# Kernel tuning notes

Measured on AMD Instinct MI355X. Metric: run time of the kernel, lower is better.

The kernel has to match this reference:

```python
import jax, jax.numpy as jnp
import numpy as np
from math import factorial

# ---------- real Clebsch-Gordan coefficients (numpy, computed once) ----------

def _cg(j1, m1, j2, m2, j3, m3):
    if m1 + m2 != m3 or not (abs(j1 - j2) <= j3 <= j1 + j2):
        return 0.0
    f = factorial
    pref = ((2 * j3 + 1) * f(j3 + j1 - j2) * f(j3 - j1 + j2) * f(j1 + j2 - j3) / f(j1 + j2 + j3 + 1)) ** 0.5
    pref *= (f(j3 + m3) * f(j3 - m3) * f(j1 - m1) * f(j1 + m1) * f(j2 - m2) * f(j2 + m2)) ** 0.5
    s = 0.0
    for k in range(0, j1 + j2 + j3 + 1):
        dn = [j1 + j2 - j3 - k, j1 - m1 - k, j2 + m2 - k, j3 - j2 + m1 + k, j3 - j1 - m2 + k]
        if any(t < 0 for t in dn):
            continue
        s += (-1) ** k / (f(k) * f(dn[0]) * f(dn[1]) * f(dn[2]) * f(dn[3]) * f(dn[4]))
    return pref * s

def _U(l):
    # complex -> real spherical-harmonic change of basis, rows = real m (-l..l)
    u = np.zeros((2 * l + 1, 2 * l + 1), dtype=complex)
    s = 1.0 / np.sqrt(2.0)
    u[l, l] = 1.0
    for m in range(1, l + 1):
        u[l + m, l + m] = (-1) ** m * s
        u[l + m, l - m] = s
        u[l - m, l - m] = 1j * s
        u[l - m, l + m] = -1j * (-1) ** m * s
    return u

def _real_cg(l1, l2, l3):
    Cc = np.zeros((2 * l1 + 1, 2 * l2 + 1, 2 * l3 + 1), dtype=complex)
    for i, m1 in enumerate(range(-l1, l1 + 1)):
        for j, m2 in enumerate(range(-l2, l2 + 1)):
            for k, m3 in enumerate(range(-l3, l3 + 1)):
                Cc[i, j, k] = _cg(l1, m1, l2, m2, l3, m3)
    Cr = np.einsum('ia,jb,kc,abc->ijk', _U(l1), _U(l2), _U(l3).conj(), Cc)
    return np.real(Cr).astype(np.float32)

C110 = _real_cg(1, 1, 0); C220 = _real_cg(2, 2, 0)
C121 = _real_cg(1, 2, 1); C211 = _real_cg(2, 1, 1); C231 = _real_cg(2, 3, 1)
C112 = _real_cg(1, 1, 2); C132 = _real_cg(1, 3, 2); C222 = _real_cg(2, 2, 2)

N_NODE, N_EDGE, F, AVG = 5000, 50000, 64, 10.0


def setup_inputs() -> dict:
    key = jax.random.key(0)
    ks = jax.random.split(key, 20)
    nrm = lambda k, sh: jax.random.normal(k, sh, dtype=jnp.float32)
    return {
        'vectors': nrm(ks[0], (N_EDGE, 3)) * 0.25,  # keep lengths mostly < r_cut=1
        'node_feats': nrm(ks[1], (N_NODE, 9 * F)),   # 64x0e + 64x1o + 64x2e
        'node_specie': jnp.zeros((N_NODE,), jnp.int32),
        'senders': jax.random.randint(ks[2], (N_EDGE,), 0, N_NODE),
        'receivers': jax.random.randint(ks[3], (N_EDGE,), 0, N_NODE),
        'Wsc0': nrm(ks[4], (1, F, F)), 'Wsc1': nrm(ks[5], (1, F, F)), 'Wsc2': nrm(ks[6], (1, F, F)),
        'Wu0': nrm(ks[7], (F, F)), 'Wu1': nrm(ks[8], (F, F)), 'Wu2': nrm(ks[9], (F, F)),
        'Wm1': nrm(ks[10], (8, 64)), 'Wm2': nrm(ks[11], (64, 64)), 'Wm3': nrm(ks[12], (64, 13 * F)),
        'Wd0': nrm(ks[13], (3 * F, 3 * F)), 'Wd1': nrm(ks[14], (5 * F, F)), 'Wd2': nrm(ks[15], (5 * F, F)),
    }


def reference(vectors, node_feats, node_specie, senders, receivers,
              Wsc0, Wsc1, Wsc2, Wu0, Wu1, Wu2, Wm1, Wm2, Wm3, Wd0, Wd1, Wd2):
    N = node_feats.shape[0]
    # radial embedding: bessel(8) * poly_envelope(5,2)  (r_cut = 1)
    x = jnp.sqrt(jnp.maximum(jnp.sum(vectors ** 2, -1), 1e-12))  # [E]
    unit = vectors / x[:, None]
    n = jnp.arange(1, 9, dtype=vectors.dtype)
    basis = jnp.sqrt(2.0) * jnp.sin(jnp.pi * n[None, :] * x[:, None]) / x[:, None]  # [E,8]
    env = jnp.where(x < 1.0, 1.0 - 28 * x ** 6 + 48 * x ** 7 - 21 * x ** 8, 0.0)
    radial = basis * env[:, None]
    # spherical harmonics l=1..3, component normalization, m = -l..l
    ux, uy, uz = unit[:, 0], unit[:, 1], unit[:, 2]
    sh1 = (3.0 ** 0.5) * jnp.stack([uy, uz, ux], -1)
    s15, s5 = 15.0 ** 0.5, 5.0 ** 0.5
    sh2 = jnp.stack([s15 * ux * uy, s15 * uy * uz, 0.5 * s5 * (3 * uz ** 2 - 1), s15 * ux * uz, 0.5 * s15 * (ux ** 2 - uy ** 2)], -1)
    c35, c105, c21, c7 = (35.0 / 8) ** 0.5, 105.0 ** 0.5, (21.0 / 8) ** 0.5, (7.0 ** 0.5) / 2
    sh3 = jnp.stack([c35 * uy * (3 * ux ** 2 - uy ** 2), c105 * ux * uy * uz, c21 * uy * (5 * uz ** 2 - 1),
                     c7 * uz * (5 * uz ** 2 - 3), c21 * ux * (5 * uz ** 2 - 1), 0.5 * c105 * uz * (ux ** 2 - uy ** 2),
                     c35 * ux * (ux ** 2 - 3 * uy ** 2)], -1)
    # split node features into irrep blocks: [N,F], [N,F,3], [N,F,5]
    f0 = node_feats[:, :F]
    f1 = node_feats[:, F:4 * F].reshape(N, F, 3)
    f2 = node_feats[:, 4 * F:9 * F].reshape(N, F, 5)
    inv_f = 1.0 / F ** 0.5
    # species-indexed skip connection (on pre-linear_up features)
    sc0 = jnp.einsum('nf,nfg->ng', f0, Wsc0[node_specie]) * inv_f
    sc1 = jnp.einsum('nfc,nfg->ngc', f1, Wsc1[node_specie]) * inv_f
    sc2 = jnp.einsum('nfc,nfg->ngc', f2, Wsc2[node_specie]) * inv_f
    # linear_up (per-irrep channel mixing)
    g0 = (f0 @ Wu0) * inv_f
    g1 = jnp.einsum('nfc,fg->ngc', f1, Wu1) * inv_f
    g2 = jnp.einsum('nfc,fg->ngc', f2, Wu2) * inv_f
    # gather sender features onto edges
    s0, s1, s2 = g0[senders], g1[senders], g2[senders]
    tp = lambda feat, sh, C: jnp.einsum('efi,ej,ijk->efk', feat, sh, jnp.asarray(C))
    # messages = concat(filtered feats, CG tensor products filtered to 0e+1o+2e)
    m0 = jnp.concatenate([s0, tp(s1, sh1, C110)[..., 0], tp(s2, sh2, C220)[..., 0]], 1)            # [E,3F]
    m1 = jnp.concatenate([s1, s0[:, :, None] * sh1[:, None, :], tp(s1, sh2, C121),
                          tp(s2, sh1, C211), tp(s2, sh3, C231)], 1)                                   # [E,5F,3]
    m2 = jnp.concatenate([s2, s0[:, :, None] * sh2[:, None, :], tp(s1, sh1, C112),
                          tp(s1, sh3, C132), tp(s2, sh2, C222)], 1)                                   # [E,5F,5]
    # edge-wise scalar MLP on radial embedding -> one gain per message irrep (13F)
    h = jax.nn.swish(radial @ Wm1 / 8.0 ** 0.5)
    h = jax.nn.swish(h @ Wm2 / 64.0 ** 0.5)
    mix = h @ Wm3 / 64.0 ** 0.5                                                                        # [E,13F]
    m0 = m0 * mix[:, :3 * F]
    m1 = m1 * mix[:, 3 * F:8 * F, None]
    m2 = m2 * mix[:, 8 * F:13 * F, None]
    # scatter-add aggregation into receivers
    inv_avg = 1.0 / AVG ** 0.5
    a0 = jax.ops.segment_sum(m0, receivers, num_segments=N) * inv_avg
    a1 = jax.ops.segment_sum(m1, receivers, num_segments=N) * inv_avg
    a2 = jax.ops.segment_sum(m2, receivers, num_segments=N) * inv_avg
    # linear_down to 3F x0e (F feats + 2F gates) + F x1o + F x2e
    d0 = a0 @ Wd0 / (3 * F) ** 0.5
    d1 = jnp.einsum('nmc,mf->nfc', a1, Wd1) / (5 * F) ** 0.5
    d2 = jnp.einsum('nmc,mf->nfc', a2, Wd2) / (5 * F) ** 0.5
    # gate nonlinearity
    x0 = jax.nn.swish(d0[:, :F])
    gates = jax.nn.swish(d0[:, F:3 * F])
    o1 = d1 * gates[:, :F, None]
    o2 = d2 * gates[:, F:2 * F, None]
    return jnp.concatenate([x0 + sc0, (o1 + sc1).reshape(N, 3 * F), (o2 + sc2).reshape(N, 5 * F)], 1)
```

## Files before the change

### kernel.cpp

```cpp
#include <hip/hip_runtime.h>
#include <math.h>

#define CG110 0
#define CG220 9
#define CG121 34
#define CG211 79
#define CG231 124
#define CG112 229
#define CG132 274
#define CG222 379
#define CGTOT 504

__device__ double dfact(int n){ double r=1.0; for(int i=2;i<=n;i++) r*=(double)i; return r; }

__device__ double cg_coeff(int j1,int m1,int j2,int m2,int j3,int m3){
  if(m1+m2!=m3) return 0.0;
  int lo = j1>j2 ? j1-j2 : j2-j1;
  if(j3 < lo || j3 > j1+j2) return 0.0;
  double pref = sqrt((double)(2*j3+1)*dfact(j3+j1-j2)*dfact(j3-j1+j2)*dfact(j1+j2-j3)/dfact(j1+j2+j3+1));
  pref *= sqrt(dfact(j3+m3)*dfact(j3-m3)*dfact(j1-m1)*dfact(j1+m1)*dfact(j2-m2)*dfact(j2+m2));
  double s=0.0;
  for(int k=0;k<=j1+j2+j3;k++){
    int d0=j1+j2-j3-k, d1=j1-m1-k, d2=j2+m2-k, d3=j3-j2+m1+k, d4=j3-j1-m2+k;
    if(d0<0||d1<0||d2<0||d3<0||d4<0) continue;
    double term = 1.0/(dfact(k)*dfact(d0)*dfact(d1)*dfact(d2)*dfact(d3)*dfact(d4));
    s += (k&1)? -term : term;
  }
  return pref*s;
}

__device__ void u_elem(int l,int i,int a,double& re,double& im){
  const double s=0.70710678118654752440;
  re=0.0; im=0.0;
  int mi=i-l, ma=a-l;
  if(mi==0){ if(ma==0) re=1.0; }
  else if(mi>0){ if(ma==mi) re=(mi&1)?-s:s; else if(ma==-mi) re=s; }
  else { int m=-mi; if(ma==mi) im=s; else if(ma==-mi) im=(m&1)?s:-s; }
}

__device__ float real_cg_elem(int l1,int l2,int l3,int ii,int jj,int kk){
  double acc=0.0;
  int alist[2]={ii, 2*l1-ii}; int na=(alist[1]==alist[0])?1:2;
  int blist[2]={jj, 2*l2-jj}; int nb=(blist[1]==blist[0])?1:2;
  int clist[2]={kk, 2*l3-kk}; int nc=(clist[1]==clist[0])?1:2;
  for(int ai=0;ai<na;ai++) for(int bi=0;bi<nb;bi++) for(int ci=0;ci<nc;ci++){
    int a=alist[ai], b=blist[bi], c=clist[ci];
    double w = cg_coeff(l1,a-l1,l2,b-l2,l3,c-l3);
    if(w==0.0) continue;
    double u1r,u1i,u2r,u2i,u3r,u3i;
    u_elem(l1,ii,a,u1r,u1i); u_elem(l2,jj,b,u2r,u2i); u_elem(l3,kk,c,u3r,u3i);
    double ar = u1r*u2r - u1i*u2i;
    double aiv= u1r*u2i + u1i*u2r;
    acc += (ar*u3r + aiv*u3i)*w;
  }
  return (float)acc;
}

__global__ void cg_init_kernel(float* __restrict__ cgbuf){
  int tid = blockIdx.x*blockDim.x + threadIdx.x;
  if(tid>=CGTOT) return;
  const int l1s[8]={1,2,1,2,2,1,1,2};
  const int l2s[8]={1,2,2,1,3,1,3,2};
  const int l3s[8]={0,0,1,1,1,2,2,2};
  const int offs[9]={CG110,CG220,CG121,CG211,CG231,CG112,CG132,CG222,CGTOT};
  int t=0;
  for(int u=0;u<8;u++){ if(tid>=offs[u] && tid<offs[u+1]){ t=u; break; } }
  int l1=l1s[t], l2=l2s[t], l3=l3s[t];
  int rem = tid - offs[t];
  int d3=2*l3+1, d2=2*l2+1;
  int k = rem % d3; int j = (rem/d3)%d2; int i = rem/(d3*d2);
  cgbuf[tid] = real_cg_elem(l1,l2,l3,i,j,k);
}


__global__ __launch_bounds__(256) void node_linear_kernel(
    const float* __restrict__ node_feats, const int* __restrict__ specie,
    const float* __restrict__ Wsc0, const float* __restrict__ Wsc1, const float* __restrict__ Wsc2,
    const float* __restrict__ Wu0,  const float* __restrict__ Wu1,  const float* __restrict__ Wu2,
    float* __restrict__ g_packed, float* __restrict__ sc_packed, int N)
{
  __shared__ float feat[576];
  int n = blockIdx.x; if(n>=N) return;
  const float4* src = (const float4*)(node_feats + (size_t)n*576);
  float4* fd = (float4*)feat;
  for(int i=threadIdx.x;i<144;i+=256) fd[i]=src[i];
  __syncthreads();
  int sp = specie[n];
  const float inv_f = 0.125f;
  for(int o=threadIdx.x; o<1152; o+=256){
    int isSc = (o>=576);
    int p = o - (isSc?576:0);
    float acc=0.f;
    if(p<64){
      const float* W = isSc ? (Wsc0 + (size_t)sp*4096) : Wu0;
      #pragma unroll 8
      for(int f=0; f<64; f++) acc += feat[f]*W[f*64+p];
    } else if(p<256){
      int q=p-64; int f,c;
      if (isSc){ f=q/3; c=q-3*f; } else { c=q>>6; f=q&63; }
      const float* W = isSc ? (Wsc1 + (size_t)sp*4096) : Wu1;
      #pragma unroll 8
      for(int fp=0; fp<64; fp++) acc += feat[64+3*fp+c]*W[fp*64+f];
    } else {
      int q=p-256; int f,c;
      if (isSc){ f=q/5; c=q-5*f; } else { c=q>>6; f=q&63; }
      const float* W = isSc ? (Wsc2 + (size_t)sp*4096) : Wu2;
      #pragma unroll 8
      for(int fp=0; fp<64; fp++) acc += feat[256+5*fp+c]*W[fp*64+f];
    }
    float* dst = isSc ? sc_packed : g_packed;
    dst[(size_t)n*576 + p] = acc*inv_f;
  }
}

__global__ __launch_bounds__(256) void node_gemm_kernel(
  const float* __restrict__ node_feats,
  const float* __restrict__ Wsc0, const float* __restrict__ Wsc1, const float* __restrict__ Wsc2,
  const float* __restrict__ Wu0,  const float* __restrict__ Wu1,  const float* __restrict__ Wu2,
  float* __restrict__ g_packed, float* __restrict__ sc_packed, int N)
{
  __shared__ float As[64][17];
  __shared__ float Bs[16][64];
  int tid = threadIdx.x;
  int tx = tid & 15, ty = tid >> 4;
  int s = blockIdx.y;
  int n0 = blockIdx.x*64;

  int sub = s % 9;
  int isSc = (s >= 9);
  int abase, astride;
  const float* W;
  if (sub == 0){ abase = 0; astride = 1; W = isSc? Wsc0 : Wu0; }
  else if (sub < 4){ int c = sub-1; abase = 64+c; astride = 3; W = isSc? Wsc1 : Wu1; }
  else { int c = sub-4; abase = 256+c; astride = 5; W = isSc? Wsc2 : Wu2; }
  int obase, ostride;
  if (isSc){ obase = abase; ostride = astride; }
  else {
    if (sub==0){ obase=0; ostride=1; }
    else if (sub<4){ obase = 64+64*(sub-1); ostride=1; }
    else { obase = 256+64*(sub-4); ostride=1; }
  }
  float* dst = isSc ? sc_packed : g_packed;

  float acc[4][4];
  #pragma unroll
  for(int i=0;i<4;i++)
    #pragma unroll
    for(int j=0;j<4;j++) acc[i][j]=0.f;

  for (int k0=0; k0<64; k0+=16){
    #pragma unroll
    for (int l=0;l<4;l++){
      int idx = tid + l*256;
      int row = idx>>4, kk = idx&15;
      int n = n0+row;
      As[row][kk] = (n<N)? node_feats[(size_t)n*576 + abase + astride*(k0+kk)] : 0.f;
    }
    #pragma unroll
    for (int l=0;l<4;l++){
      int idx = tid + l*256;
      int kk = idx>>6, j = idx&63;
      Bs[kk][j] = W[(k0+kk)*64 + j];
    }
    __syncthreads();
    #pragma unroll
    for (int kk=0; kk<16; kk++){
      float av[4];
      #pragma unroll
      for(int i=0;i<4;i++) av[i] = As[ty*4+i][kk];
      float4 bv = *(const float4*)&Bs[kk][tx*4];
      #pragma unroll
      for(int i=0;i<4;i++){
        acc[i][0] += av[i]*bv.x; acc[i][1] += av[i]*bv.y;
        acc[i][2] += av[i]*bv.z; acc[i][3] += av[i]*bv.w;
      }
    }
    __syncthreads();
  }
  const float scale = 0.125f;
  #pragma unroll
  for(int i=0;i<4;i++){
    int n = n0 + ty*4+i;
    if (n>=N) continue;
    #pragma unroll
    for(int j=0;j<4;j++){
      int f = tx*4+j;
      dst[(size_t)n*576 + obase + ostride*f] = acc[i][j]*scale;
    }
  }
}

__global__ void count_kernel(const int* __restrict__ recv, int* __restrict__ counts, int E){
  int e = blockIdx.x*256 + threadIdx.x;
  if(e<E) atomicAdd(&counts[recv[e]],1);
}

__global__ __launch_bounds__(1024) void scan_kernel(const int* __restrict__ counts,
                                                    int* __restrict__ offsets,
                                                    int* __restrict__ cursor, int n){
  __shared__ int tmp[1024];
  int tid = threadIdx.x;
  int per = (n + 1023)/1024;
  int base = tid*per;
  int s = 0;
  for(int i=0;i<per;i++){ int idx=base+i; if(idx<n) s += counts[idx]; }
  tmp[tid]=s; __syncthreads();
  for(int off=1; off<1024; off<<=1){
    int v = (tid>=off)? tmp[tid-off] : 0;
    __syncthreads();
    tmp[tid]+=v;
    __syncthreads();
  }
  int run = (tid==0)? 0 : tmp[tid-1];
  for(int i=0;i<per;i++){
    int idx=base+i;
    if(idx<n){ offsets[idx]=run; cursor[idx]=run; run += counts[idx]; }
  }
  if(tid==1023) offsets[n]=tmp[1023];
}

__global__ void scatter_kernel(const int* __restrict__ recv, int* __restrict__ cursor,
                               int* __restrict__ edge_list, int E){
  int e = blockIdx.x*256 + threadIdx.x;
  if(e<E){ int pos=atomicAdd(&cursor[recv[e]],1); edge_list[pos]=e; }
}

__global__ __launch_bounds__(256) void geom_kernel(
  const float* __restrict__ vectors, const int* __restrict__ edge_list,
  const int* __restrict__ senders,
  float* __restrict__ radbuf, float* __restrict__ shbuf, int* __restrict__ spos, int E)
{
  int pos = blockIdx.x*256 + threadIdx.x;
  if (pos >= E) return;
  int e = edge_list[pos];
  spos[pos] = senders[e];
  float vx=vectors[e*3], vy=vectors[e*3+1], vz=vectors[e*3+2];
  float x2 = vx*vx+vy*vy+vz*vz;
  float x  = sqrtf(fmaxf(x2, 1e-12f));
  float inv= 1.f/x;
  float ux=vx*inv, uy=vy*inv, uz=vz*inv;
  float env = 0.f;
  if(x<1.f){
    float x3=x*x*x; float x6=x3*x3; float x7=x6*x; float x8=x7*x;
    env = 1.f-28.f*x6+48.f*x7-21.f*x8;
  }
  float* rb = radbuf + (size_t)pos*8;
  #pragma unroll
  for(int nn=1;nn<=8;nn++)
    rb[nn-1] = 1.4142135623730951f * sinf(3.14159265358979323846f*(float)nn*x)*inv*env;
  float sh[16];
  const float s3=1.7320508075688772f;
  sh[0]=s3*uy; sh[1]=s3*uz; sh[2]=s3*ux;
  const float s15=3.872983346207417f, s5=2.23606797749979f;
  sh[3]=s15*ux*uy; sh[4]=s15*uy*uz;
  sh[5]=0.5f*s5*(3.f*uz*uz-1.f);
  sh[6]=s15*ux*uz; sh[7]=0.5f*s15*(ux*ux-uy*uy);
  const float c35=2.091650066335189f, c105=10.246950765959598f;
  const float c21=1.620185174601965f, c7=1.3228756555322954f;
  sh[8] =c35*uy*(3.f*ux*ux-uy*uy);
  sh[9] =c105*ux*uy*uz;
  sh[10]=c21*uy*(5.f*uz*uz-1.f);
  sh[11]=c7*uz*(5.f*uz*uz-3.f);
  sh[12]=c21*ux*(5.f*uz*uz-1.f);
  sh[13]=0.5f*c105*uz*(ux*ux-uy*uy);
  sh[14]=c35*ux*(ux*ux-3.f*uy*uy);
  sh[15]=0.f;
  float* sb = shbuf + (size_t)pos*16;
  #pragma unroll
  for(int k=0;k<16;k++) sb[k]=sh[k];
}

__global__ __launch_bounds__(256) void wtab_kernel(
  const float* __restrict__ shbuf, const float* __restrict__ cgbuf,
  float* __restrict__ wtabbuf, int E)
{
  __shared__ float cgs[504];
  for(int i=threadIdx.x;i<504;i+=256) cgs[i]=cgbuf[i];
  __syncthreads();
  long long t = (long long)blockIdx.x*256 + threadIdx.x;
  if (t >= (long long)E*104) return;
  int pos = (int)(t/104), idx = (int)(t - (long long)pos*104);
  const float* sh = shbuf + (size_t)pos*16;
  float v = 0.f;
  if (idx < 3){
    int i=idx;
    #pragma unroll
    for(int j=0;j<3;j++) v += sh[j]*cgs[CG110+i*3+j];
  } else if (idx < 8){
    int i=idx-3;
    #pragma unroll
    for(int j=0;j<5;j++) v += sh[3+j]*cgs[CG220+i*5+j];
  } else if (idx < 17){
    int r=idx-8; int i=r/3, c=r-3*i;
    #pragma unroll
    for(int j=0;j<5;j++) v += sh[3+j]*cgs[CG121+(i*5+j)*3+c];
  } else if (idx < 32){
    int r=idx-17; int i=r/3, c=r-3*i;
    #pragma unroll
    for(int j=0;j<3;j++) v += sh[j]*cgs[CG211+(i*3+j)*3+c];
  } else if (idx < 47){
    int r=idx-32; int i=r/3, c=r-3*i;
    #pragma unroll
    for(int j=0;j<7;j++) v += sh[8+j]*cgs[CG231+(i*7+j)*3+c];
  } else if (idx < 62){
    int r=idx-47; int i=r/5, c=r-5*i;
    #pragma unroll
    for(int j=0;j<3;j++) v += sh[j]*cgs[CG112+(i*3+j)*5+c];
  } else if (idx < 77){
    int r=idx-62; int i=r/5, c=r-5*i;
    #pragma unroll
    for(int j=0;j<7;j++) v += sh[8+j]*cgs[CG132+(i*7+j)*5+c];
  } else if (idx < 102){
    int r=idx-77; int i=r/5, c=r-5*i;
    #pragma unroll
    for(int j=0;j<5;j++) v += sh[3+j]*cgs[CG222+(i*5+j)*5+c];
  }
  wtabbuf[t] = v;
}

__global__ __launch_bounds__(256) void h12_kernel(
  const float* __restrict__ radbuf, const float* __restrict__ Wm1,
  const float* __restrict__ Wm2, float* __restrict__ h2buf, int E)
{
  __shared__ float rloc[4][8];
  __shared__ float h1loc[4][64];
  int tid=threadIdx.x;
  int pos0 = blockIdx.x*4;
  if (tid<32){
    int le=tid>>3, i=tid&7;
    int p=pos0+le;
    rloc[le][i] = (p<E)? radbuf[(size_t)p*8+i] : 0.f;
  }
  __syncthreads();
  int le=tid>>6, j=tid&63;
  float a=0.f;
  #pragma unroll
  for(int i=0;i<8;i++) a += rloc[le][i]*Wm1[i*64+j];
  a *= 0.3535533905932738f;
  h1loc[le][j] = a/(1.f+expf(-a));
  __syncthreads();
  float b=0.f;
  #pragma unroll 16
  for(int i=0;i<64;i++) b += h1loc[le][i]*Wm2[i*64+j];
  b *= 0.125f;
  int p=pos0+le;
  if (p<E) h2buf[(size_t)p*64+j] = b/(1.f+expf(-b));
}

__global__ __launch_bounds__(256) void mix_gemm_kernel(
  const float* __restrict__ h2buf, const float* __restrict__ Wm3,
  float* __restrict__ mixbuf, int posLo, int cnt)
{
  __shared__ float As[64][17];
  __shared__ float Bs[16][64];
  int tid=threadIdx.x; int tx=tid&15, ty=tid>>4;
  int r0 = blockIdx.x*64;
  int c0 = blockIdx.y*64;
  float acc[4][4];
  #pragma unroll
  for(int i=0;i<4;i++)
    #pragma unroll
    for(int j=0;j<4;j++) acc[i][j]=0.f;
  for(int k0=0;k0<64;k0+=16){
    #pragma unroll
    for(int l=0;l<4;l++){
      int idx=tid+l*256; int row=idx>>4, kk=idx&15;
      int r=r0+row;
      As[row][kk] = (r<cnt)? h2buf[(size_t)(posLo+r)*64 + k0+kk] : 0.f;
    }
    #pragma unroll
    for(int l=0;l<4;l++){
      int idx=tid+l*256; int kk=idx>>6, j=idx&63;
      Bs[kk][j] = Wm3[(size_t)(k0+kk)*832 + c0 + j];
    }
    __syncthreads();
    #pragma unroll
    for(int kk=0;kk<16;kk++){
      float av[4];
      #pragma unroll
      for(int i=0;i<4;i++) av[i]=As[ty*4+i][kk];
      float4 bv = *(const float4*)&Bs[kk][tx*4];
      #pragma unroll
      for(int i=0;i<4;i++){
        acc[i][0]+=av[i]*bv.x; acc[i][1]+=av[i]*bv.y;
        acc[i][2]+=av[i]*bv.z; acc[i][3]+=av[i]*bv.w;
      }
    }
    __syncthreads();
  }
  #pragma unroll
  for(int i=0;i<4;i++){
    int r=r0+ty*4+i;
    if(r>=cnt) continue;
    float4 o;
    o.x=acc[i][0]*0.125f; o.y=acc[i][1]*0.125f;
    o.z=acc[i][2]*0.125f; o.w=acc[i][3]*0.125f;
    *(float4*)&mixbuf[(size_t)r*832 + c0 + tx*4] = o;
  }
}

__global__ __launch_bounds__(256) void node_accum_kernel(
  const float* __restrict__ g_packed, const int* __restrict__ spos,
  const float* __restrict__ shbuf, const float* __restrict__ wtabbuf,
  const float* __restrict__ mixbuf, const int* __restrict__ offsets,
  float* __restrict__ a_packed, int posLo, int posHi, int N)
{
  __shared__ float accs[2752];
  __shared__ float wt_l[4][112];
  int n = blockIdx.x; if (n>=N) return;
  int tid = threadIdx.x, wave = tid>>6, lane = tid&63;
  int e0 = offsets[n], e1 = offsets[n+1];
  int a0 = e0>posLo? e0:posLo;
  int a1 = e1<posHi? e1:posHi;
  bool first = (posLo==0);
  if (!first && a0>=a1) return;

  for (int i=tid;i<2752;i+=256) accs[i]=0.f;

  float racc[43];
  #pragma unroll
  for(int k=0;k<43;k++) racc[k]=0.f;

  for (int pos=a0+wave; pos<a1; pos+=4){
    int rp = pos - posLo;
    const float* wsrc = wtabbuf + (size_t)pos*104;
    wt_l[wave][lane] = wsrc[lane];
    if (lane<40) wt_l[wave][64+lane] = wsrc[64+lane];
    else if (lane<48) wt_l[wave][64+lane] = shbuf[(size_t)pos*16 + (lane-40)];
    const float* g = g_packed + (size_t)spos[pos]*576;
    const float* mx = mixbuf + (size_t)rp*832;
    float s0  = g[lane];
    float s10 = g[64+lane],  s11 = g[128+lane], s12 = g[192+lane];
    float s20 = g[256+lane], s21 = g[320+lane], s22 = g[384+lane],
          s23 = g[448+lane], s24 = g[512+lane];
    const float* W = wt_l[wave];
    const float* shv = W + 104;
    racc[0] += s0*mx[lane];
    racc[1] += (s10*W[0]+s11*W[1]+s12*W[2])*mx[64+lane];
    racc[2] += (s20*W[3]+s21*W[4]+s22*W[5]+s23*W[6]+s24*W[7])*mx[128+lane];
    {
      float m0_=mx[192+lane], m1_=mx[256+lane], m2_=mx[320+lane],
            m3_=mx[384+lane], m4_=mx[448+lane];
      float p1v[3]={s10,s11,s12};
      #pragma unroll
      for(int c=0;c<3;c++){
        float v2 = s10*W[8+c]+s11*W[11+c]+s12*W[14+c];
        float v3 = s20*W[17+c]+s21*W[20+c]+s22*W[23+c]+s23*W[26+c]+s24*W[29+c];
        float v4 = s20*W[32+c]+s21*W[35+c]+s22*W[38+c]+s23*W[41+c]+s24*W[44+c];
        racc[3+c*5+0] += p1v[c]*m0_;
        racc[3+c*5+1] += s0*shv[c]*m1_;
        racc[3+c*5+2] += v2*m2_;
        racc[3+c*5+3] += v3*m3_;
        racc[3+c*5+4] += v4*m4_;
      }
    }
    {
      float n0_=mx[512+lane], n1_=mx[576+lane], n2_=mx[640+lane],
            n3_=mx[704+lane], n4_=mx[768+lane];
      float p2v[5]={s20,s21,s22,s23,s24};
      #pragma unroll
      for(int c=0;c<5;c++){
        float v2 = s10*W[47+c]+s11*W[52+c]+s12*W[57+c];
        float v3 = s10*W[62+c]+s11*W[67+c]+s12*W[72+c];
        float v4 = s20*W[77+c]+s21*W[82+c]+s22*W[87+c]+s23*W[92+c]+s24*W[97+c];
        racc[18+c*5+0] += p2v[c]*n0_;
        racc[18+c*5+1] += s0*shv[3+c]*n1_;
        racc[18+c*5+2] += v2*n2_;
        racc[18+c*5+3] += v3*n3_;
        racc[18+c*5+4] += v4*n4_;
      }
    }
  }
  __syncthreads();
  for (int w=0; w<4; w++){
    if (wave==w){
      accs[lane]     += racc[0];
      accs[64+lane]  += racc[1];
      accs[128+lane] += racc[2];
      #pragma unroll
      for(int c=0;c<3;c++)
        #pragma unroll
        for(int p=0;p<5;p++)
          accs[192+c*320+p*64+lane] += racc[3+c*5+p];
      #pragma unroll
      for(int c=0;c<5;c++)
        #pragma unroll
        for(int p=0;p<5;p++)
          accs[1152+c*320+p*64+lane] += racc[18+c*5+p];
    }
    __syncthreads();
  }
  if (first){
    for (int i=tid;i<2752;i+=256) a_packed[(size_t)n*2752+i] = accs[i];
  } else {
    for (int i=tid;i<2752;i+=256) a_packed[(size_t)n*2752+i] += accs[i];
  }
}

__global__ __launch_bounds__(256) void out_gemm_kernel(
  const float* __restrict__ A, const float* __restrict__ Wd0,
  const float* __restrict__ Wd1, const float* __restrict__ Wd2,
  float* __restrict__ dbuf, int N)
{
  __shared__ float As[32][17];
  __shared__ float Bs[16][64];
  int tid = threadIdx.x;
  int tx = tid & 15, ty = tid >> 4;
  int s = blockIdx.y;
  int n0 = blockIdx.x*32;

  int abase, K, obase, bcol0, bstride;
  const float* W;
  float scale;
  if (s < 3){
    abase = 0; K = 192; W = Wd0; bcol0 = 64*s; bstride = 192;
    obase = 64*s;
    scale = 0.02282177322938192f;
  } else if (s < 6){
    int c = s-3;
    abase = 192+320*c; K = 320; W = Wd1; bcol0 = 0; bstride = 64;
    obase = 192+64*c;
    scale = 0.017677669529663688f;
  } else {
    int c = s-6;
    abase = 1152+320*c; K = 320; W = Wd2; bcol0 = 0; bstride = 64;
    obase = 384+64*c;
    scale = 0.017677669529663688f;
  }

  float acc[2][4];
  #pragma unroll
  for(int i=0;i<2;i++)
    #pragma unroll
    for(int j=0;j<4;j++) acc[i][j]=0.f;

  for (int k0=0; k0<K; k0+=16){
    #pragma unroll
    for (int l=0;l<2;l++){
      int idx = tid + l*256;
      int row = idx>>4, kk = idx&15;
      int n = n0+row;
      As[row][kk] = (n<N)? A[(size_t)n*2752 + abase + k0+kk] : 0.f;
    }
    #pragma unroll
    for (int l=0;l<4;l++){
      int idx = tid + l*256;
      int kk = idx>>6, j = idx&63;
      Bs[kk][j] = W[(size_t)(k0+kk)*bstride + bcol0 + j];
    }
    __syncthreads();
    #pragma unroll
    for (int kk=0; kk<16; kk++){
      float av[2];
      av[0] = As[ty*2][kk]; av[1] = As[ty*2+1][kk];
      float4 bv = *(const float4*)&Bs[kk][tx*4];
      #pragma unroll
      for(int i=0;i<2;i++){
        acc[i][0] += av[i]*bv.x; acc[i][1] += av[i]*bv.y;
        acc[i][2] += av[i]*bv.z; acc[i][3] += av[i]*bv.w;
      }
    }
    __syncthreads();
  }
  #pragma unroll
  for(int i=0;i<2;i++){
    int n = n0 + ty*2+i;
    if (n>=N) continue;
    #pragma unroll
    for(int j=0;j<4;j++){
      int col = tx*4+j;
      dbuf[(size_t)n*704 + obase + col] = acc[i][j]*scale;
    }
  }
}

__global__ __launch_bounds__(256) void epilogue_kernel(
  const float* __restrict__ dbuf, const float* __restrict__ sc_packed,
  float* __restrict__ out, int N)
{
  int n = blockIdx.x; if(n>=N) return;
  const float* d = dbuf + (size_t)n*704;
  const float* sc = sc_packed + (size_t)n*576;
  float* o = out + (size_t)n*576;
  for (int p=threadIdx.x; p<576; p+=256){
    float v;
    if (p<64){
      float x = d[p];
      v = x/(1.f+expf(-x)) + sc[p];
    } else if (p<256){
      int r = p-64; int f = r/3, c = r-3*f;
      float g = d[64+f]; g = g/(1.f+expf(-g));
      v = d[192+64*c+f]*g + sc[p];
    } else {
      int r = p-256; int f = r/5, c = r-5*f;
      float g = d[128+f]; g = g/(1.f+expf(-g));
      v = d[384+64*c+f]*g + sc[p];
    }
    o[p] = v;
  }
}

extern "C" void kernel_launch(void* const* d_in, const int* in_sizes, int n_in,
                              void* d_out, int out_size, void* d_ws, size_t ws_size,
                              hipStream_t stream)
{
  const float* vectors    =(const float*)d_in[0];
  const float* node_feats =(const float*)d_in[1];
  const int*   node_specie=(const int*)  d_in[2];
  const int*   senders    =(const int*)  d_in[3];
  const int*   receivers  =(const int*)  d_in[4];
  const float* Wsc0=(const float*)d_in[5];
  const float* Wsc1=(const float*)d_in[6];
  const float* Wsc2=(const float*)d_in[7];
  const float* Wu0 =(const float*)d_in[8];
  const float* Wu1 =(const float*)d_in[9];
  const float* Wu2 =(const float*)d_in[10];
  const float* Wm1 =(const float*)d_in[11];
  const float* Wm2 =(const float*)d_in[12];
  const float* Wm3 =(const float*)d_in[13];
  const float* Wd0 =(const float*)d_in[14];
  const float* Wd1 =(const float*)d_in[15];
  const float* Wd2 =(const float*)d_in[16];
  float* out = (float*)d_out;

  int E = in_sizes[0]/3;
  int N = in_sizes[1]/576;
  int nspec = in_sizes[5]/4096;

  float* cgbuf     = (float*)d_ws;
  float* g_packed  = cgbuf + 512;
  float* sc_packed = g_packed  + (size_t)N*576;
  float* a_packed  = sc_packed + (size_t)N*576;
  float* radbuf    = a_packed + (size_t)N*2752;
  float* shbuf     = radbuf + (size_t)E*8;
  float* wtabbuf   = shbuf + (size_t)E*16;
  float* h2buf     = wtabbuf + (size_t)E*104;
  int*   counts    = (int*)(h2buf + (size_t)E*64);
  int*   offsets   = counts + N;
  int*   cursor    = offsets + (N+1);
  int*   edge_list = cursor + N;
  int*   spos      = edge_list + E;
  size_t used_bytes = (size_t)((char*)(spos + E) - (char*)d_ws);
  used_bytes = (used_bytes + 255) & ~(size_t)255;
  size_t avail = (ws_size > used_bytes) ? (ws_size - used_bytes) : 0;
  long long cap = (long long)(avail / (832u*4u));
  if (cap > E) cap = E;
  cap = (cap/8)*8;
  if (cap < 8) cap = 8;
  float* mixbuf = (float*)((char*)d_ws + used_bytes);
  float* dbuf   = mixbuf;

  hipMemsetAsync(counts, 0, (size_t)N*sizeof(int), stream);
  cg_init_kernel<<<2,256,0,stream>>>(cgbuf);
  if (nspec == 1){
    dim3 grid((N+63)/64, 18);
    node_gemm_kernel<<<grid,256,0,stream>>>(node_feats,Wsc0,Wsc1,Wsc2,Wu0,Wu1,Wu2,
                                            g_packed,sc_packed,N);
  } else {
    node_linear_kernel<<<N,256,0,stream>>>(node_feats,node_specie,Wsc0,Wsc1,Wsc2,Wu0,Wu1,Wu2,
                                           g_packed,sc_packed,N);
  }
  count_kernel<<<(E+255)/256,256,0,stream>>>(receivers,counts,E);
  scan_kernel<<<1,1024,0,stream>>>(counts,offsets,cursor,N);
  scatter_kernel<<<(E+255)/256,256,0,stream>>>(receivers,cursor,edge_list,E);
  geom_kernel<<<(E+255)/256,256,0,stream>>>(vectors,edge_list,senders,radbuf,shbuf,spos,E);
  {
    long long tasks = (long long)E*104;
    wtab_kernel<<<(unsigned)((tasks+255)/256),256,0,stream>>>(shbuf,cgbuf,wtabbuf,E);
  }
  h12_kernel<<<(E+3)/4,256,0,stream>>>(radbuf,Wm1,Wm2,h2buf,E);

  for (long long lo=0; lo<E; lo+=cap){
    long long hi = lo + cap; if (hi > E) hi = E;
    int cnt = (int)(hi - lo);
    {
      dim3 grid((cnt+63)/64, 13);
      mix_gemm_kernel<<<grid,256,0,stream>>>(h2buf,Wm3,mixbuf,(int)lo,cnt);
    }
    node_accum_kernel<<<N,256,0,stream>>>(g_packed,spos,shbuf,wtabbuf,mixbuf,offsets,
                                          a_packed,(int)lo,(int)hi,N);
  }

  {
    dim3 grid((N+31)/32, 11);
    out_gemm_kernel<<<grid,256,0,stream>>>(a_packed,Wd0,Wd1,Wd2,dbuf,N);
  }
  epilogue_kernel<<<N,256,0,stream>>>(dbuf,sc_packed,out,N);
}
```

Baseline: 513.3 us.

## Fuse radial MLP into geometry kernel and repack mix buffer per lane

Computes the two-layer radial MLP per edge inside the geometry kernel, so the separate h12 kernel and the radial buffer round-trip go away. h2 is now stored feature-major so the mix GEMM reads it coalesced. The mix buffer is re-laid out so each lane's 13 gains are contiguous (stride 16) and node_accum can load them with float4 instead of 13 strided loads. In exchange, each geometry thread holds a 64-float accumulator and does 8x64 plus 64x64 FMAs with uniform weight loads, which adds register pressure, and the mix GEMM now does scattered scalar stores. The chunk cap is limited to 16384 edges.

```diff
diff --git a/kernel.cpp b/kernel.cpp
--- a/kernel.cpp
+++ b/kernel.cpp
@@ -225,15 +225,17 @@
   if(e<E){ int pos=atomicAdd(&cursor[recv[e]],1); edge_list[pos]=e; }
 }
 
-__global__ __launch_bounds__(256) void geom_kernel(
+__global__ __launch_bounds__(256) void geomh_kernel(
   const float* __restrict__ vectors, const int* __restrict__ edge_list,
   const int* __restrict__ senders,
-  float* __restrict__ radbuf, float* __restrict__ shbuf, int* __restrict__ spos, int E)
+  const float* __restrict__ Wm1, const float* __restrict__ Wm2,
+  float* __restrict__ shbuf, float* __restrict__ h2buf, int* __restrict__ spos, int E)
 {
   int pos = blockIdx.x*256 + threadIdx.x;
-  if (pos >= E) return;
-  int e = edge_list[pos];
-  spos[pos] = senders[e];
+  bool valid = pos < E;
+  int pp = valid ? pos : (E-1);
+  int e = edge_list[pp];
+  if (valid) spos[pos] = senders[e];
   float vx=vectors[e*3], vy=vectors[e*3+1], vz=vectors[e*3+2];
   float x2 = vx*vx+vy*vy+vz*vz;
   float x  = sqrtf(fmaxf(x2, 1e-12f));
@@ -244,30 +246,54 @@
     float x3=x*x*x; float x6=x3*x3; float x7=x6*x; float x8=x7*x;
     env = 1.f-28.f*x6+48.f*x7-21.f*x8;
   }
-  float* rb = radbuf + (size_t)pos*8;
+  float rad[8];
   #pragma unroll
   for(int nn=1;nn<=8;nn++)
-    rb[nn-1] = 1.4142135623730951f * sinf(3.14159265358979323846f*(float)nn*x)*inv*env;
-  float sh[16];
-  const float s3=1.7320508075688772f;
-  sh[0]=s3*uy; sh[1]=s3*uz; sh[2]=s3*ux;
-  const float s15=3.872983346207417f, s5=2.23606797749979f;
-  sh[3]=s15*ux*uy; sh[4]=s15*uy*uz;
-  sh[5]=0.5f*s5*(3.f*uz*uz-1.f);
-  sh[6]=s15*ux*uz; sh[7]=0.5f*s15*(ux*ux-uy*uy);
-  const float c35=2.091650066335189f, c105=10.246950765959598f;
-  const float c21=1.620185174601965f, c7=1.3228756555322954f;
-  sh[8] =c35*uy*(3.f*ux*ux-uy*uy);
-  sh[9] =c105*ux*uy*uz;
-  sh[10]=c21*uy*(5.f*uz*uz-1.f);
-  sh[11]=c7*uz*(5.f*uz*uz-3.f);
-  sh[12]=c21*ux*(5.f*uz*uz-1.f);
-  sh[13]=0.5f*c105*uz*(ux*ux-uy*uy);
-  sh[14]=c35*ux*(ux*ux-3.f*uy*uy);
-  sh[15]=0.f;
-  float* sb = shbuf + (size_t)pos*16;
-  #pragma unroll
-  for(int k=0;k<16;k++) sb[k]=sh[k];
+    rad[nn-1] = 1.4142135623730951f * sinf(3.14159265358979323846f*(float)nn*x)*inv*env;
+  {
+    float sh[16];
+    const float s3=1.7320508075688772f;
+    sh[0]=s3*uy; sh[1]=s3*uz; sh[2]=s3*ux;
+    const float s15=3.872983346207417f, s5=2.23606797749979f;
+    sh[3]=s15*ux*uy; sh[4]=s15*uy*uz;
+    sh[5]=0.5f*s5*(3.f*uz*uz-1.f);
+    sh[6]=s15*ux*uz; sh[7]=0.5f*s15*(ux*ux-uy*uy);
+    const float c35=2.091650066335189f, c105=10.246950765959598f;
+    const float c21=1.620185174601965f, c7=1.3228756555322954f;
+    sh[8] =c35*uy*(3.f*ux*ux-uy*uy);
+    sh[9] =c105*ux*uy*uz;
+    sh[10]=c21*uy*(5.f*uz*uz-1.f);
+    sh[11]=c7*uz*(5.f*uz*uz-3.f);
+    sh[12]=c21*ux*(5.f*uz*uz-1.f);
+    sh[13]=0.5f*c105*uz*(ux*ux-uy*uy);
+    sh[14]=c35*ux*(ux*ux-3.f*uy*uy);
+    sh[15]=0.f;
+    if (valid){
+      float* sb = shbuf + (size_t)pos*16;
+      #pragma unroll
+      for(int k=0;k<16;k++) sb[k]=sh[k];
+    }
+  }
+  float h2a[64];
+  #pragma unroll
+  for(int j=0;j<64;j++) h2a[j]=0.f;
+  for(int i=0;i<64;i++){
+    float a=0.f;
+    #pragma unroll
+    for(int r=0;r<8;r++) a += rad[r]*Wm1[r*64+i];
+    a *= 0.3535533905932738f;
+    float h1 = a/(1.f+expf(-a));
+    const float* wrow = Wm2 + i*64;
+    #pragma unroll
+    for(int j=0;j<64;j++) h2a[j] += h1*wrow[j];
+  }
+  if (valid){
+    #pragma unroll
+    for(int j=0;j<64;j++){
+      float b = h2a[j]*0.125f;
+      h2buf[(size_t)j*E + pos] = b/(1.f+expf(-b));
+    }
+  }
 }
 
 __global__ __launch_bounds__(256) void wtab_kernel(
@@ -318,44 +344,16 @@
   wtabbuf[t] = v;
 }
 
-__global__ __launch_bounds__(256) void h12_kernel(
-  const float* __restrict__ radbuf, const float* __restrict__ Wm1,
-  const float* __restrict__ Wm2, float* __restrict__ h2buf, int E)
-{
-  __shared__ float rloc[4][8];
-  __shared__ float h1loc[4][64];
-  int tid=threadIdx.x;
-  int pos0 = blockIdx.x*4;
-  if (tid<32){
-    int le=tid>>3, i=tid&7;
-    int p=pos0+le;
-    rloc[le][i] = (p<E)? radbuf[(size_t)p*8+i] : 0.f;
-  }
-  __syncthreads();
-  int le=tid>>6, j=tid&63;
-  float a=0.f;
-  #pragma unroll
-  for(int i=0;i<8;i++) a += rloc[le][i]*Wm1[i*64+j];
-  a *= 0.3535533905932738f;
-  h1loc[le][j] = a/(1.f+expf(-a));
-  __syncthreads();
-  float b=0.f;
-  #pragma unroll 16
-  for(int i=0;i<64;i++) b += h1loc[le][i]*Wm2[i*64+j];
-  b *= 0.125f;
-  int p=pos0+le;
-  if (p<E) h2buf[(size_t)p*64+j] = b/(1.f+expf(-b));
-}
-
 __global__ __launch_bounds__(256) void mix_gemm_kernel(
   const float* __restrict__ h2buf, const float* __restrict__ Wm3,
-  float* __restrict__ mixbuf, int posLo, int cnt)
+  float* __restrict__ mixbuf, int posLo, int cnt, int E)
 {
   __shared__ float As[64][17];
   __shared__ float Bs[16][64];
   int tid=threadIdx.x; int tx=tid&15, ty=tid>>4;
   int r0 = blockIdx.x*64;
-  int c0 = blockIdx.y*64;
+  int s  = blockIdx.y;
+  int c0 = s*64;
   float acc[4][4];
   #pragma unroll
   for(int i=0;i<4;i++)
@@ -364,9 +362,9 @@
   for(int k0=0;k0<64;k0+=16){
     #pragma unroll
     for(int l=0;l<4;l++){
-      int idx=tid+l*256; int row=idx>>4, kk=idx&15;
+      int idx=tid+l*256; int kk=idx>>6, row=idx&63;
       int r=r0+row;
-      As[row][kk] = (r<cnt)? h2buf[(size_t)(posLo+r)*64 + k0+kk] : 0.f;
+      As[row][kk] = (r<cnt)? h2buf[(size_t)(k0+kk)*E + posLo + r] : 0.f;
     }
     #pragma unroll
     for(int l=0;l<4;l++){
@@ -392,10 +390,11 @@
   for(int i=0;i<4;i++){
     int r=r0+ty*4+i;
     if(r>=cnt) continue;
-    float4 o;
-    o.x=acc[i][0]*0.125f; o.y=acc[i][1]*0.125f;
-    o.z=acc[i][2]*0.125f; o.w=acc[i][3]*0.125f;
-    *(float4*)&mixbuf[(size_t)r*832 + c0 + tx*4] = o;
+    #pragma unroll
+    for(int j=0;j<4;j++){
+      int f = tx*4+j;
+      mixbuf[(size_t)r*1024 + f*16 + s] = acc[i][j]*0.125f;
+    }
   }
 }
 
@@ -428,19 +427,22 @@
     if (lane<40) wt_l[wave][64+lane] = wsrc[64+lane];
     else if (lane<48) wt_l[wave][64+lane] = shbuf[(size_t)pos*16 + (lane-40)];
     const float* g = g_packed + (size_t)spos[pos]*576;
-    const float* mx = mixbuf + (size_t)rp*832;
+    const float* mx = mixbuf + (size_t)rp*1024 + (lane<<4);
+    float4 mA = *(const float4*)(mx);
+    float4 mB = *(const float4*)(mx+4);
+    float4 mC = *(const float4*)(mx+8);
+    float  mD = mx[12];
     float s0  = g[lane];
     float s10 = g[64+lane],  s11 = g[128+lane], s12 = g[192+lane];
     float s20 = g[256+lane], s21 = g[320+lane], s22 = g[384+lane],
           s23 = g[448+lane], s24 = g[512+lane];
     const float* W = wt_l[wave];
     const float* shv = W + 104;
-    racc[0] += s0*mx[lane];
-    racc[1] += (s10*W[0]+s11*W[1]+s12*W[2])*mx[64+lane];
-    racc[2] += (s20*W[3]+s21*W[4]+s22*W[5]+s23*W[6]+s24*W[7])*mx[128+lane];
+    racc[0] += s0*mA.x;
+    racc[1] += (s10*W[0]+s11*W[1]+s12*W[2])*mA.y;
+    racc[2] += (s20*W[3]+s21*W[4]+s22*W[5]+s23*W[6]+s24*W[7])*mA.z;
     {
-      float m0_=mx[192+lane], m1_=mx[256+lane], m2_=mx[320+lane],
-            m3_=mx[384+lane], m4_=mx[448+lane];
+      float m0_=mA.w, m1_=mB.x, m2_=mB.y, m3_=mB.z, m4_=mB.w;
       float p1v[3]={s10,s11,s12};
       #pragma unroll
       for(int c=0;c<3;c++){
@@ -455,8 +457,7 @@
       }
     }
     {
-      float n0_=mx[512+lane], n1_=mx[576+lane], n2_=mx[640+lane],
-            n3_=mx[704+lane], n4_=mx[768+lane];
+      float n0_=mC.x, n1_=mC.y, n2_=mC.z, n3_=mC.w, n4_=mD;
       float p2v[5]={s20,s21,s22,s23,s24};
       #pragma unroll
       for(int c=0;c<5;c++){
@@ -631,8 +632,7 @@
   float* g_packed  = cgbuf + 512;
   float* sc_packed = g_packed  + (size_t)N*576;
   float* a_packed  = sc_packed + (size_t)N*576;
-  float* radbuf    = a_packed + (size_t)N*2752;
-  float* shbuf     = radbuf + (size_t)E*8;
+  float* shbuf     = a_packed + (size_t)N*2752;
   float* wtabbuf   = shbuf + (size_t)E*16;
   float* h2buf     = wtabbuf + (size_t)E*104;
   int*   counts    = (int*)(h2buf + (size_t)E*64);
@@ -643,8 +643,9 @@
   size_t used_bytes = (size_t)((char*)(spos + E) - (char*)d_ws);
   used_bytes = (used_bytes + 255) & ~(size_t)255;
   size_t avail = (ws_size > used_bytes) ? (ws_size - used_bytes) : 0;
-  long long cap = (long long)(avail / (832u*4u));
-  if (cap > E) cap = E;
+  long long cap = (long long)(avail / (1024u*4u));
+  if (cap > 16384) cap = 16384;
+  if (cap > E) cap = ((long long)E + 7) & ~7ll;
   cap = (cap/8)*8;
   if (cap < 8) cap = 8;
   float* mixbuf = (float*)((char*)d_ws + used_bytes);
@@ -663,19 +664,19 @@
   count_kernel<<<(E+255)/256,256,0,stream>>>(receivers,counts,E);
   scan_kernel<<<1,1024,0,stream>>>(counts,offsets,cursor,N);
   scatter_kernel<<<(E+255)/256,256,0,stream>>>(receivers,cursor,edge_list,E);
-  geom_kernel<<<(E+255)/256,256,0,stream>>>(vectors,edge_list,senders,radbuf,shbuf,spos,E);
+  geomh_kernel<<<(E+255)/256,256,0,stream>>>(vectors,edge_list,senders,Wm1,Wm2,
+                                             shbuf,h2buf,spos,E);
   {
     long long tasks = (long long)E*104;
     wtab_kernel<<<(unsigned)((tasks+255)/256),256,0,stream>>>(shbuf,cgbuf,wtabbuf,E);
   }
-  h12_kernel<<<(E+3)/4,256,0,stream>>>(radbuf,Wm1,Wm2,h2buf,E);
 
   for (long long lo=0; lo<E; lo+=cap){
     long long hi = lo + cap; if (hi > E) hi = E;
     int cnt = (int)(hi - lo);
     {
       dim3 grid((cnt+63)/64, 13);
-      mix_gemm_kernel<<<grid,256,0,stream>>>(h2buf,Wm3,mixbuf,(int)lo,cnt);
+      mix_gemm_kernel<<<grid,256,0,stream>>>(h2buf,Wm3,mixbuf,(int)lo,cnt,E);
     }
     node_accum_kernel<<<N,256,0,stream>>>(g_packed,spos,shbuf,wtabbuf,mixbuf,offsets,
                                           a_packed,(int)lo,(int)hi,N);
```

Measured after the change: 1.048 ms. 104% more time.
